# Optimization experiments

Hardware: AMD Instinct MI355X
Metric: run time of the kernel (lower is better)

The kernel has to match this reference:

```python
import jax, jax.numpy as jnp
import numpy as np

B, T, D, U = 32, 2048, 512, 512


def setup_inputs() -> dict:
    key = jax.random.key(0)
    ks = jax.random.split(key, 6)
    scale = 0.05
    return {
        "values": jax.random.normal(ks[0], (B, T, D), dtype=jnp.float32),
        "query": jax.random.normal(ks[1], (B, D), dtype=jnp.float32),
        "W1_w": jax.random.normal(ks[2], (D, U), dtype=jnp.float32) * scale,
        "W1_b": jnp.zeros((U,), dtype=jnp.float32),
        "W2_w": jax.random.normal(ks[3], (D, U), dtype=jnp.float32) * scale,
        "W2_b": jnp.zeros((U,), dtype=jnp.float32),
        "V_w": jax.random.normal(ks[4], (U, 1), dtype=jnp.float32) * scale,
        "V_b": jnp.zeros((1,), dtype=jnp.float32),
    }


def reference(values, query, W1_w, W1_b, W2_w, W2_b, V_w, V_b):
    # values: [B, T, D]; query: [B, D]
    proj_v = jnp.einsum("btd,du->btu", values, W1_w) + W1_b          # [B, T, U]
    proj_q = (query @ W2_w + W2_b)[:, None, :]                        # [B, 1, U]
    score = jnp.tanh(proj_v + proj_q) @ V_w + V_b                     # [B, T, 1]
    attention_weights = jax.nn.softmax(score, axis=1)                 # [B, T, 1]
    context_vector = jnp.sum(attention_weights * values, axis=1)      # [B, D]
    return context_vector, attention_weights
```

## Files before the change

### kernel.cpp

```cpp
#include <hip/hip_runtime.h>
#include <hip/hip_bf16.h>
#include <stdint.h>


#define B_DIM 32
#define T_DIM 2048
#define D_DIM 512
#define U_DIM 512
#define M_DIM (B_DIM * T_DIM)

typedef short bf16x8 __attribute__((ext_vector_type(8)));
typedef float f32x4 __attribute__((ext_vector_type(4)));

__device__ __forceinline__ float fast_tanh(float x) {
    float e = __expf(2.0f * x);
    return 1.0f - __fdividef(2.0f, e + 1.0f);
}

__device__ __forceinline__ short bf16r(float x) {
    unsigned u = __float_as_uint(x);
    u += 0x7fffu + ((u >> 16) & 1u);
    return (short)(u >> 16);
}

__device__ __forceinline__ bf16x8 pack8(float4 a, float4 b) {
    union { __hip_bfloat162 h[4]; bf16x8 v; } u;
    u.h[0] = __float22bfloat162_rn(make_float2(a.x, a.y));
    u.h[1] = __float22bfloat162_rn(make_float2(a.z, a.w));
    u.h[2] = __float22bfloat162_rn(make_float2(b.x, b.y));
    u.h[3] = __float22bfloat162_rn(make_float2(b.z, b.w));
    return u.v;
}

__device__ __forceinline__ void g2lds16(const void* g, void* lds) {
    auto gp = reinterpret_cast<const __attribute__((address_space(1))) unsigned int*>(
        reinterpret_cast<uintptr_t>(g));
    auto lp = reinterpret_cast<__attribute__((address_space(3))) unsigned int*>(
        (unsigned int)(uintptr_t)lds);
    __builtin_amdgcn_global_load_lds(gp, lp, 16, 0, 0);
}


__global__ void prep_kernel(const float* __restrict__ W1_w,
                            const float* __restrict__ W1_b,
                            const float* __restrict__ W2_w,
                            const float* __restrict__ W2_b,
                            const float* __restrict__ query,
                            unsigned short* __restrict__ W1T,
                            float* __restrict__ qb) {
    __shared__ float red[256];
    const int tid = threadIdx.x;
    if (blockIdx.x < 128) {
        int n = blockIdx.x * 256 + tid;
        int uu    = n & 255;
        int kc    = (n >> 8) & 3;
        int kstep = (n >> 10) & 15;
        int ut    = n >> 14;
        int u  = ut * 256 + uu;
        int k0 = kstep * 32 + kc * 8;
        bf16x8 pk;
#pragma unroll
        for (int j = 0; j < 8; ++j)
            pk[j] = bf16r(W1_w[(size_t)(k0 + j) * U_DIM + u]);
        ((bf16x8*)W1T)[n] = pk;
    } else {
        int bid = blockIdx.x - 128;
        int b  = bid >> 3;
        int ug = bid & 7;
        int u  = ug * 64 + (tid & 63);
        int dq = tid >> 6;
        const float* q  = query + b * D_DIM + dq * 128;
        const float* w2 = W2_w + (size_t)(dq * 128) * U_DIM + u;
        float acc = 0.f;
#pragma unroll 8
        for (int d = 0; d < 128; ++d)
            acc += q[d] * w2[(size_t)d * U_DIM];
        red[tid] = acc;
        __syncthreads();
        if (tid < 64) {
            qb[b * U_DIM + u] = red[tid] + red[tid + 64] + red[tid + 128]
                              + red[tid + 192] + W2_b[u] + W1_b[u];
        }
    }
}

__global__ __launch_bounds__(512, 4) void score_kernel(
        const float* __restrict__ values,
        const unsigned short* __restrict__ W1T,
        const float* __restrict__ qb,
        const float* __restrict__ Vw,
        float* __restrict__ sP) {
    __shared__ __align__(16) unsigned char smem[2][16384];

    const int tid  = threadIdx.x;
    const int lane = tid & 63;
    const int w    = tid >> 6;
    const int l15  = lane & 15;
    const int quad = lane >> 4;
    const int wr   = w >> 1;
    const int wc   = w & 1;
    const int ut    = blockIdx.x & 1;
    const int mb    = (blockIdx.x >> 1) * 128;
    const int b     = mb >> 11;

    const float* arow0 = values + (size_t)(mb + wr * 32 + l15) * D_DIM + quad * 8;
    const float* arow1 = arow0 + 16 * D_DIM;
    const unsigned short* wsrc = W1T + (size_t)ut * 16 * 8192;

#pragma unroll
    for (int i = 0; i < 2; ++i) {
        int unit = i * 512 + w * 64 + lane;
        g2lds16(wsrc + (size_t)unit * 8, smem[0] + unit * 16);
    }

    f32x4 acc[2][8] = {};

    for (int ks = 0; ks < 16; ++ks) {
        float4 a00 = *(const float4*)(arow0 + ks * 32);
        float4 a01 = *(const float4*)(arow0 + ks * 32 + 4);
        float4 a10 = *(const float4*)(arow1 + ks * 32);
        float4 a11 = *(const float4*)(arow1 + ks * 32 + 4);

        __syncthreads();

        if (ks < 15) {
            const unsigned short* src = wsrc + (size_t)(ks + 1) * 8192;
            unsigned char* nbuf = smem[(ks + 1) & 1];
#pragma unroll
            for (int i = 0; i < 2; ++i) {
                int unit = i * 512 + w * 64 + lane;
                g2lds16(src + (size_t)unit * 8, nbuf + unit * 16);
            }
        }

        bf16x8 a0 = pack8(a00, a01);
        bf16x8 a1 = pack8(a10, a11);
        const unsigned char* bbase =
            smem[ks & 1] + (size_t)(quad * 256 + wc * 128 + l15) * 16;
#pragma unroll
        for (int ui = 0; ui < 8; ++ui) {
            bf16x8 bf = *(const bf16x8*)(bbase + ui * 256);
            acc[0][ui] = __builtin_amdgcn_mfma_f32_16x16x32_bf16(a0, bf, acc[0][ui], 0, 0, 0);
            acc[1][ui] = __builtin_amdgcn_mfma_f32_16x16x32_bf16(a1, bf, acc[1][ui], 0, 0, 0);
        }
    }

    const int ub = ut * 256 + wc * 128 + l15;
    float sm[2][4] = {};
#pragma unroll
    for (int ui = 0; ui < 8; ++ui) {
        const int u = ub + ui * 16;
        const float qv = qb[b * U_DIM + u];
        const float vw = Vw[u];
#pragma unroll
        for (int mt = 0; mt < 2; ++mt)
#pragma unroll
            for (int r = 0; r < 4; ++r)
                sm[mt][r] += fast_tanh(acc[mt][ui][r] + qv) * vw;
    }
#pragma unroll
    for (int mt = 0; mt < 2; ++mt)
#pragma unroll
        for (int r = 0; r < 4; ++r) {
            float v = sm[mt][r];
            v += __shfl_xor(v, 1, 64);
            v += __shfl_xor(v, 2, 64);
            v += __shfl_xor(v, 4, 64);
            v += __shfl_xor(v, 8, 64);
            sm[mt][r] = v;
        }
    if (l15 == 0) {
        const int slice = ut * 2 + wc;
#pragma unroll
        for (int mt = 0; mt < 2; ++mt)
#pragma unroll
            for (int r = 0; r < 4; ++r)
                sP[slice * M_DIM + mb + wr * 32 + mt * 16 + quad * 4 + r] = sm[mt][r];
    }
}

__global__ void softmax_kernel(const float* __restrict__ sP,
                               float* __restrict__ out) {
    const int b = blockIdx.x;
    const int tid = threadIdx.x;

    float v[8];
    float mx = -1e30f;
#pragma unroll
    for (int i = 0; i < 8; ++i) {
        int m = b * T_DIM + i * 256 + tid;
        v[i] = sP[m] + sP[M_DIM + m] + sP[2 * M_DIM + m] + sP[3 * M_DIM + m];
        mx = fmaxf(mx, v[i]);
    }
#pragma unroll
    for (int off = 1; off < 64; off <<= 1)
        mx = fmaxf(mx, __shfl_xor(mx, off, 64));
    __shared__ float redm[4];
    if ((tid & 63) == 0) redm[tid >> 6] = mx;
    __syncthreads();
    mx = fmaxf(fmaxf(redm[0], redm[1]), fmaxf(redm[2], redm[3]));

    float sum = 0.f;
#pragma unroll
    for (int i = 0; i < 8; ++i) {
        v[i] = __expf(v[i] - mx);
        sum += v[i];
    }
#pragma unroll
    for (int off = 1; off < 64; off <<= 1)
        sum += __shfl_xor(sum, off, 64);
    __shared__ float reds[4];
    if ((tid & 63) == 0) reds[tid >> 6] = sum;
    __syncthreads();
    sum = reds[0] + reds[1] + reds[2] + reds[3];

    const float inv = 1.0f / sum;
#pragma unroll
    for (int i = 0; i < 8; ++i)
        out[B_DIM * D_DIM + b * T_DIM + i * 256 + tid] = v[i] * inv;
}

__global__ void context_kernel(const float* __restrict__ values,
                               const float* __restrict__ weights,
                               float* __restrict__ P) {
    __shared__ float sw[64];
    __shared__ float red[512];
    const int tc = blockIdx.x;
    const int b  = blockIdx.y;
    const int tid = threadIdx.x;
    const int d4 = tid & 127;
    const int th = tid >> 7;

    if (tid < 64) sw[tid] = weights[b * T_DIM + tc * 64 + tid];
    __syncthreads();

    const float4* vb = (const float4*)(values + ((size_t)b * T_DIM + tc * 64) * D_DIM) + d4;
    float4 acc = {0.f, 0.f, 0.f, 0.f};
#pragma unroll 8
    for (int i = th; i < 64; i += 2) {
        float wv = sw[i];
        float4 vv = vb[(size_t)i * 128];
        acc.x += wv * vv.x; acc.y += wv * vv.y;
        acc.z += wv * vv.z; acc.w += wv * vv.w;
    }
    if (th == 1) ((float4*)red)[d4] = acc;
    __syncthreads();
    if (th == 0) {
        float4 o = ((float4*)red)[d4];
        acc.x += o.x; acc.y += o.y; acc.z += o.z; acc.w += o.w;
        *(float4*)(P + ((size_t)(b * 32 + tc)) * 512 + d4 * 4) = acc;
    }
}

__global__ void reduce_kernel(const float* __restrict__ P,
                              float* __restrict__ ctx) {
    const int g = blockIdx.x * 256 + threadIdx.x;
    const int b = g >> 9, d = g & 511;
    float s = 0.f;
#pragma unroll
    for (int tc = 0; tc < 32; ++tc)
        s += P[((size_t)(b * 32 + tc)) * 512 + d];
    ctx[g] = s;
}

extern "C" void kernel_launch(void* const* d_in, const int* in_sizes, int n_in,
                              void* d_out, int out_size, void* d_ws, size_t ws_size,
                              hipStream_t stream) {
    const float* values = (const float*)d_in[0];
    const float* query  = (const float*)d_in[1];
    const float* W1_w   = (const float*)d_in[2];
    const float* W1_b   = (const float*)d_in[3];
    const float* W2_w   = (const float*)d_in[4];
    const float* W2_b   = (const float*)d_in[5];
    const float* V_w    = (const float*)d_in[6];

    float* out = (float*)d_out;

    unsigned char* ws = (unsigned char*)d_ws;
    unsigned short* W1T = (unsigned short*)(ws);
    float* qb = (float*)(ws + 524288);
    float* sP = (float*)(ws + 524288 + 65536);
    float* P  = (float*)(ws + 524288 + 65536 + 1048576);

    prep_kernel<<<384, 256, 0, stream>>>(W1_w, W1_b, W2_w, W2_b, query, W1T, qb);
    score_kernel<<<1024, 512, 0, stream>>>(values, W1T, qb, V_w, sP);
    softmax_kernel<<<B_DIM, 256, 0, stream>>>(sP, out);
    context_kernel<<<dim3(32, B_DIM), 256, 0, stream>>>(values, out + B_DIM * D_DIM, P);
    reduce_kernel<<<64, 256, 0, stream>>>(P, out);
}
```

Before: 283.0 us.

## Triple-buffer W1 tiles in LDS and prefetch value rows one step ahead

The score GEMM main loop becomes a fully unrolled, templated pipeline. W1 tiles are loaded into a three-deep LDS ring two steps ahead, and the fp32 value rows for the next k-step are prefetched into ping-pong registers. Explicit vmcnt waits and sched_barriers replace the per-iteration __syncthreads, leaving a single s_barrier per step. The goal is to hide global load latency behind the MFMAs, at the cost of 48KB of LDS per block, which may lower the number of resident blocks per CU.

```diff
diff --git a/kernel.cpp b/kernel.cpp
--- a/kernel.cpp
+++ b/kernel.cpp
@@ -23,12 +23,12 @@
     return (short)(u >> 16);
 }
 
-__device__ __forceinline__ bf16x8 pack8(float4 a, float4 b) {
+__device__ __forceinline__ bf16x8 pack8v(f32x4 a, f32x4 b) {
     union { __hip_bfloat162 h[4]; bf16x8 v; } u;
-    u.h[0] = __float22bfloat162_rn(make_float2(a.x, a.y));
-    u.h[1] = __float22bfloat162_rn(make_float2(a.z, a.w));
-    u.h[2] = __float22bfloat162_rn(make_float2(b.x, b.y));
-    u.h[3] = __float22bfloat162_rn(make_float2(b.z, b.w));
+    u.h[0] = __float22bfloat162_rn(make_float2(a[0], a[1]));
+    u.h[1] = __float22bfloat162_rn(make_float2(a[2], a[3]));
+    u.h[2] = __float22bfloat162_rn(make_float2(b[0], b[1]));
+    u.h[3] = __float22bfloat162_rn(make_float2(b[2], b[3]));
     return u.v;
 }
 
@@ -84,13 +84,59 @@
     }
 }
 
+template <int KS>
+__device__ __forceinline__ void score_step(
+        const unsigned short* __restrict__ wsrc,
+        unsigned char* __restrict__ sm0,
+        int tid,
+        const float* __restrict__ arow0,
+        const float* __restrict__ arow1,
+        const unsigned char* __restrict__ bb,
+        f32x4& c00, f32x4& c01, f32x4& c10, f32x4& c11,
+        f32x4& n00, f32x4& n01, f32x4& n10, f32x4& n11,
+        f32x4 (&acc)[2][8]) {
+    __builtin_amdgcn_s_barrier();
+    __builtin_amdgcn_sched_barrier(0);
+    if constexpr (KS <= 13) {
+        const unsigned short* src = wsrc + (size_t)(KS + 2) * 8192;
+        unsigned char* nbuf = sm0 + ((KS + 2) % 3) * 16384;
+        g2lds16(src + (size_t)tid * 8,        nbuf + tid * 16);
+        g2lds16(src + 4096 + (size_t)tid * 8, nbuf + 8192 + tid * 16);
+    }
+    __builtin_amdgcn_sched_barrier(0);
+    if constexpr (KS <= 14) {
+        n00 = *(const f32x4*)(arow0 + (KS + 1) * 32);
+        n01 = *(const f32x4*)(arow0 + (KS + 1) * 32 + 4);
+        n10 = *(const f32x4*)(arow1 + (KS + 1) * 32);
+        n11 = *(const f32x4*)(arow1 + (KS + 1) * 32 + 4);
+    }
+    __builtin_amdgcn_sched_barrier(0);
+    if constexpr (KS <= 13) {
+        asm volatile("s_waitcnt vmcnt(10)" ::: "memory");
+    } else if constexpr (KS == 14) {
+        asm volatile("s_waitcnt vmcnt(8)" ::: "memory");
+    }
+    __builtin_amdgcn_sched_barrier(0);
+
+    bf16x8 a0 = pack8v(c00, c01);
+    bf16x8 a1 = pack8v(c10, c11);
+    const unsigned char* bbk = bb + (KS % 3) * 16384;
+#pragma unroll
+    for (int ui = 0; ui < 8; ++ui) {
+        bf16x8 bf = *(const bf16x8*)(bbk + ui * 256);
+        acc[0][ui] = __builtin_amdgcn_mfma_f32_16x16x32_bf16(a0, bf, acc[0][ui], 0, 0, 0);
+        acc[1][ui] = __builtin_amdgcn_mfma_f32_16x16x32_bf16(a1, bf, acc[1][ui], 0, 0, 0);
+    }
+    __builtin_amdgcn_sched_barrier(0);
+}
+
 __global__ __launch_bounds__(512, 4) void score_kernel(
         const float* __restrict__ values,
         const unsigned short* __restrict__ W1T,
         const float* __restrict__ qb,
         const float* __restrict__ Vw,
         float* __restrict__ sP) {
-    __shared__ __align__(16) unsigned char smem[2][16384];
+    __shared__ __align__(16) unsigned char smem[3][16384];
 
     const int tid  = threadIdx.x;
     const int lane = tid & 63;
@@ -99,51 +145,49 @@
     const int quad = lane >> 4;
     const int wr   = w >> 1;
     const int wc   = w & 1;
-    const int ut    = blockIdx.x & 1;
-    const int mb    = (blockIdx.x >> 1) * 128;
-    const int b     = mb >> 11;
+    const int ut   = blockIdx.x & 1;
+    const int mb   = (blockIdx.x >> 1) * 128;
+    const int b    = mb >> 11;
 
     const float* arow0 = values + (size_t)(mb + wr * 32 + l15) * D_DIM + quad * 8;
     const float* arow1 = arow0 + 16 * D_DIM;
     const unsigned short* wsrc = W1T + (size_t)ut * 16 * 8192;
-
-#pragma unroll
-    for (int i = 0; i < 2; ++i) {
-        int unit = i * 512 + w * 64 + lane;
-        g2lds16(wsrc + (size_t)unit * 8, smem[0] + unit * 16);
-    }
-
+    unsigned char* sm0 = &smem[0][0];
+    const unsigned char* bb = sm0 + (size_t)(quad * 256 + wc * 128 + l15) * 16;
+
+    g2lds16(wsrc + (size_t)tid * 8,        sm0 + tid * 16);
+    g2lds16(wsrc + 4096 + (size_t)tid * 8, sm0 + 8192 + tid * 16);
+    __builtin_amdgcn_sched_barrier(0);
+    g2lds16(wsrc + 8192 + (size_t)tid * 8,        sm0 + 16384 + tid * 16);
+    g2lds16(wsrc + 8192 + 4096 + (size_t)tid * 8, sm0 + 16384 + 8192 + tid * 16);
+    __builtin_amdgcn_sched_barrier(0);
+    f32x4 cA00 = *(const f32x4*)(arow0);
+    f32x4 cA01 = *(const f32x4*)(arow0 + 4);
+    f32x4 cA10 = *(const f32x4*)(arow1);
+    f32x4 cA11 = *(const f32x4*)(arow1 + 4);
+    __builtin_amdgcn_sched_barrier(0);
+    asm volatile("s_waitcnt vmcnt(6)" ::: "memory");
+    __builtin_amdgcn_sched_barrier(0);
+
+    f32x4 cB00, cB01, cB10, cB11;
     f32x4 acc[2][8] = {};
 
-    for (int ks = 0; ks < 16; ++ks) {
-        float4 a00 = *(const float4*)(arow0 + ks * 32);
-        float4 a01 = *(const float4*)(arow0 + ks * 32 + 4);
-        float4 a10 = *(const float4*)(arow1 + ks * 32);
-        float4 a11 = *(const float4*)(arow1 + ks * 32 + 4);
-
-        __syncthreads();
-
-        if (ks < 15) {
-            const unsigned short* src = wsrc + (size_t)(ks + 1) * 8192;
-            unsigned char* nbuf = smem[(ks + 1) & 1];
-#pragma unroll
-            for (int i = 0; i < 2; ++i) {
-                int unit = i * 512 + w * 64 + lane;
-                g2lds16(src + (size_t)unit * 8, nbuf + unit * 16);
-            }
-        }
-
-        bf16x8 a0 = pack8(a00, a01);
-        bf16x8 a1 = pack8(a10, a11);
-        const unsigned char* bbase =
-            smem[ks & 1] + (size_t)(quad * 256 + wc * 128 + l15) * 16;
-#pragma unroll
-        for (int ui = 0; ui < 8; ++ui) {
-            bf16x8 bf = *(const bf16x8*)(bbase + ui * 256);
-            acc[0][ui] = __builtin_amdgcn_mfma_f32_16x16x32_bf16(a0, bf, acc[0][ui], 0, 0, 0);
-            acc[1][ui] = __builtin_amdgcn_mfma_f32_16x16x32_bf16(a1, bf, acc[1][ui], 0, 0, 0);
-        }
-    }
+    score_step<0 >(wsrc, sm0, tid, arow0, arow1, bb, cA00, cA01, cA10, cA11, cB00, cB01, cB10, cB11, acc);
+    score_step<1 >(wsrc, sm0, tid, arow0, arow1, bb, cB00, cB01, cB10, cB11, cA00, cA01, cA10, cA11, acc);
+    score_step<2 >(wsrc, sm0, tid, arow0, arow1, bb, cA00, cA01, cA10, cA11, cB00, cB01, cB10, cB11, acc);
+    score_step<3 >(wsrc, sm0, tid, arow0, arow1, bb, cB00, cB01, cB10, cB11, cA00, cA01, cA10, cA11, acc);
+    score_step<4 >(wsrc, sm0, tid, arow0, arow1, bb, cA00, cA01, cA10, cA11, cB00, cB01, cB10, cB11, acc);
+    score_step<5 >(wsrc, sm0, tid, arow0, arow1, bb, cB00, cB01, cB10, cB11, cA00, cA01, cA10, cA11, acc);
+    score_step<6 >(wsrc, sm0, tid, arow0, arow1, bb, cA00, cA01, cA10, cA11, cB00, cB01, cB10, cB11, acc);
+    score_step<7 >(wsrc, sm0, tid, arow0, arow1, bb, cB00, cB01, cB10, cB11, cA00, cA01, cA10, cA11, acc);
+    score_step<8 >(wsrc, sm0, tid, arow0, arow1, bb, cA00, cA01, cA10, cA11, cB00, cB01, cB10, cB11, acc);
+    score_step<9 >(wsrc, sm0, tid, arow0, arow1, bb, cB00, cB01, cB10, cB11, cA00, cA01, cA10, cA11, acc);
+    score_step<10>(wsrc, sm0, tid, arow0, arow1, bb, cA00, cA01, cA10, cA11, cB00, cB01, cB10, cB11, acc);
+    score_step<11>(wsrc, sm0, tid, arow0, arow1, bb, cB00, cB01, cB10, cB11, cA00, cA01, cA10, cA11, acc);
+    score_step<12>(wsrc, sm0, tid, arow0, arow1, bb, cA00, cA01, cA10, cA11, cB00, cB01, cB10, cB11, acc);
+    score_step<13>(wsrc, sm0, tid, arow0, arow1, bb, cB00, cB01, cB10, cB11, cA00, cA01, cA10, cA11, acc);
+    score_step<14>(wsrc, sm0, tid, arow0, arow1, bb, cA00, cA01, cA10, cA11, cB00, cB01, cB10, cB11, acc);
+    score_step<15>(wsrc, sm0, tid, arow0, arow1, bb, cB00, cB01, cB10, cB11, cA00, cA01, cA10, cA11, acc);
 
     const int ub = ut * 256 + wc * 128 + l15;
     float sm[2][4] = {};
@@ -175,7 +219,7 @@
         for (int mt = 0; mt < 2; ++mt)
 #pragma unroll
             for (int r = 0; r < 4; ++r)
-                sP[slice * M_DIM + mb + wr * 32 + mt * 16 + quad * 4 + r] = sm[mt][r];
+                sP[(size_t)slice * M_DIM + mb + wr * 32 + mt * 16 + quad * 4 + r] = sm[mt][r];
     }
 }
 
```

Result: no change. 283.7 us (+0.2%).
